# Performance work log

Hardware: AMD Instinct MI355X
Metric: run time of the kernel (lower is better)

Reference implementation:

```python
import jax, jax.numpy as jnp
import numpy as np

HEADS = 4
DIM_HEAD = 32


def setup_inputs() -> dict:
    key = jax.random.key(0)
    k1, k2, k3, k4 = jax.random.split(key, 4)
    x = jax.random.normal(k1, (2, 64, 48, 48, 48), dtype=jnp.float32)
    # 1x1x1 conv weights collapse to plain channel-mixing matrices
    w_qkv = jax.random.normal(k2, (384, 64), dtype=jnp.float32) * 0.05  # [3*heads*dh, dim]
    w_out = jax.random.normal(k3, (64, 128), dtype=jnp.float32) * 0.05  # [dim, heads*dh]
    b_out = jax.random.normal(k4, (64,), dtype=jnp.float32) * 0.05
    return {"x": x, "w_qkv": w_qkv, "w_out": w_out, "b_out": b_out}


def reference(x, w_qkv, w_out, b_out):
    b, c, D, H, W = x.shape
    N = D * H * W
    x_flat = x.reshape(b, c, N)
    # 1x1 conv == channel matmul: [b, 3*heads*dh, N]
    qkv = jnp.einsum('oc,bcn->bon', w_qkv, x_flat)
    # channel order: (qkv, heads, dh)
    qkv = qkv.reshape(b, 3, HEADS, DIM_HEAD, N)
    q, k, v = qkv[:, 0], qkv[:, 1], qkv[:, 2]
    k = jax.nn.softmax(k, axis=-1)  # softmax over the token axis N
    context = jnp.einsum('bhdn,bhen->bhde', k, v)   # [b, h, dh, dh]
    out = jnp.einsum('bhde,bhdn->bhen', context, q)  # [b, h, dh, N]
    out = out.reshape(b, HEADS * DIM_HEAD, N)
    y = jnp.einsum('oc,bcn->bon', w_out, out) + b_out[None, :, None]
    return y.reshape(b, c, D, H, W)
```

## Files before the change

### kernel.cpp

```cpp
#include <hip/hip_runtime.h>


#define C_IN 64
#define NREP 16

typedef __attribute__((ext_vector_type(8))) short short8;
typedef __attribute__((ext_vector_type(4))) float f32x4;

static __device__ __forceinline__ unsigned short f2bf(float f) {
    union { float f; unsigned u; } x; x.f = f;
    return (unsigned short)((x.u + 0x7fffu + ((x.u >> 16) & 1u)) >> 16);
}

__global__ __launch_bounds__(256)
void transpose_kernel(const float* __restrict__ x,
                      unsigned short* __restrict__ xT,
                      int N, int bbase)
{
    __shared__ float Xs[64][65];
    const int by = blockIdx.y;
    const int b  = by + bbase;
    const int t  = threadIdx.x;
    const int n0 = blockIdx.x * 64;

    const float* xb = x + (size_t)b * C_IN * N;
    #pragma unroll
    for (int i = 0; i < 4; ++i) {
        int slot = i * 256 + t;
        int c = slot >> 4, nq = slot & 15;
        float4 v = *(const float4*)(xb + (size_t)c * N + n0 + nq * 4);
        Xs[c][nq * 4 + 0] = v.x; Xs[c][nq * 4 + 1] = v.y;
        Xs[c][nq * 4 + 2] = v.z; Xs[c][nq * 4 + 3] = v.w;
    }
    __syncthreads();

    const int n = t >> 2, q = t & 3;
    unsigned out[8];
    #pragma unroll
    for (int i = 0; i < 8; ++i) {
        float lo = Xs[q * 16 + 2 * i][n], hi = Xs[q * 16 + 2 * i + 1][n];
        out[i] = (unsigned)f2bf(lo) | ((unsigned)f2bf(hi) << 16);
    }
    unsigned short* dst = xT + ((size_t)by * N + n0 + n) * 64 + q * 16;
    *(uint4*)(dst)     = *(uint4*)&out[0];
    *(uint4*)(dst + 8) = *(uint4*)&out[4];
}

__global__ __launch_bounds__(256, 3)
void kv_ctx_mfma(const unsigned short* __restrict__ xT,
                 const float* __restrict__ w_qkv,
                 float* __restrict__ ctx_acc,
                 float* __restrict__ s_acc,
                 int N, int bbase)
{
    __shared__ __align__(16) unsigned short PV[4][2][32][72];

    const int by  = blockIdx.y;
    const int b   = by + bbase;
    const int t   = threadIdx.x;
    const int w   = t >> 6;
    const int l   = t & 63;
    const int l15 = l & 15;
    const int lg  = l >> 4;
    const int rep = blockIdx.x & (NREP - 1);

    const int n_blk = blockIdx.x * 256;

    short8 Wf[4][2];
    #pragma unroll
    for (int nt = 0; nt < 4; ++nt) {
        const int row = (nt < 2) ? (128 + w * 32 + nt * 16 + l15)
                                 : (256 + w * 32 + (nt - 2) * 16 + l15);
        const float* wr = w_qkv + (size_t)row * C_IN;
        #pragma unroll
        for (int s = 0; s < 2; ++s) {
            #pragma unroll
            for (int j = 0; j < 8; ++j)
                Wf[nt][s][j] = (short)f2bf(wr[s * 32 + lg * 8 + j]);
        }
    }

    f32x4 acc2[2][2];
    #pragma unroll
    for (int dt = 0; dt < 2; ++dt)
        #pragma unroll
        for (int et = 0; et < 2; ++et)
            acc2[dt][et] = (f32x4){0.f, 0.f, 0.f, 0.f};
    float s_loc[2] = {0.f, 0.f};

    for (int it = 0; it < 4; ++it) {
        const int nb = n_blk + it * 64;
        const unsigned short* xr = xT + ((size_t)by * N + nb) * 64;

        short8 Af[4][2];
        #pragma unroll
        for (int mt = 0; mt < 4; ++mt)
            #pragma unroll
            for (int s = 0; s < 2; ++s)
                Af[mt][s] = *(const short8*)(xr + (size_t)(mt * 16 + l15) * 64
                                             + s * 32 + lg * 8);

        #pragma unroll
        for (int mt = 0; mt < 4; ++mt) {
            #pragma unroll
            for (int nt = 0; nt < 4; ++nt) {
                f32x4 a = (f32x4){0.f, 0.f, 0.f, 0.f};
                a = __builtin_amdgcn_mfma_f32_16x16x32_bf16(Af[mt][0], Wf[nt][0], a, 0, 0, 0);
                a = __builtin_amdgcn_mfma_f32_16x16x32_bf16(Af[mt][1], Wf[nt][1], a, 0, 0, 0);
                const int nl = mt * 16 + lg * 4;
                if (nt < 2) {
                    float e0 = __expf(a[0]), e1 = __expf(a[1]);
                    float e2 = __expf(a[2]), e3 = __expf(a[3]);
                    s_loc[nt] += (e0 + e1) + (e2 + e3);
                    uint2 p;
                    p.x = (unsigned)f2bf(e0) | ((unsigned)f2bf(e1) << 16);
                    p.y = (unsigned)f2bf(e2) | ((unsigned)f2bf(e3) << 16);
                    *(uint2*)&PV[w][0][nt * 16 + l15][nl] = p;
                } else {
                    uint2 p;
                    p.x = (unsigned)f2bf(a[0]) | ((unsigned)f2bf(a[1]) << 16);
                    p.y = (unsigned)f2bf(a[2]) | ((unsigned)f2bf(a[3]) << 16);
                    *(uint2*)&PV[w][1][(nt - 2) * 16 + l15][nl] = p;
                }
            }
        }

        #pragma unroll
        for (int ns = 0; ns < 2; ++ns) {
            short8 A2[2], B2[2];
            #pragma unroll
            for (int dt = 0; dt < 2; ++dt)
                A2[dt] = *(const short8*)&PV[w][0][dt * 16 + l15][ns * 32 + lg * 8];
            #pragma unroll
            for (int et = 0; et < 2; ++et)
                B2[et] = *(const short8*)&PV[w][1][et * 16 + l15][ns * 32 + lg * 8];
            #pragma unroll
            for (int dt = 0; dt < 2; ++dt)
                #pragma unroll
                for (int et = 0; et < 2; ++et)
                    acc2[dt][et] = __builtin_amdgcn_mfma_f32_16x16x32_bf16(
                        A2[dt], B2[et], acc2[dt][et], 0, 0, 0);
        }
    }

    float* cb = ctx_acc + (((size_t)b * NREP + rep) * 128 + w * 32) * 32;
    #pragma unroll
    for (int dt = 0; dt < 2; ++dt)
        #pragma unroll
        for (int et = 0; et < 2; ++et)
            #pragma unroll
            for (int r = 0; r < 4; ++r)
                atomicAdd(&cb[(dt * 16 + lg * 4 + r) * 32 + et * 16 + l15],
                          acc2[dt][et][r]);

    #pragma unroll
    for (int nt = 0; nt < 2; ++nt) {
        float s = s_loc[nt];
        s += __shfl_xor(s, 16);
        s += __shfl_xor(s, 32);
        if (lg == 0)
            atomicAdd(&s_acc[((size_t)b * NREP + rep) * 128 + w * 32 + nt * 16 + l15], s);
    }
}

__global__ __launch_bounds__(256)
void finalize_kernel(const float* __restrict__ ctx_acc,
                     const float* __restrict__ s_acc,
                     const float* __restrict__ w_qkv,
                     const float* __restrict__ w_out,
                     unsigned short* __restrict__ wf_bf)
{
    const int b = blockIdx.y;
    const int s = blockIdx.x;
    const int t = threadIdx.x;

    __shared__ float Wq[128][64];
    __shared__ float Ctx[128][36];
    __shared__ float Tt[128][68];
    __shared__ float WoS[8][128];
    __shared__ float Sinv[128];

    #pragma unroll
    for (int i = 0; i < 8; ++i) {
        int idx = i * 1024 + t * 4;
        *(float4*)&Wq[idx >> 6][idx & 63] = *(const float4*)(w_qkv + idx);
    }
    {
        int idx = t * 4;
        int o = idx >> 7, he = idx & 127;
        *(float4*)&WoS[o][he] = *(const float4*)(w_out + (size_t)(s * 8 + o) * 128 + he);
    }
    if (t < 128) {
        float ssum = 0.f;
        #pragma unroll
        for (int rep = 0; rep < NREP; ++rep)
            ssum += s_acc[((size_t)b * NREP + rep) * 128 + t];
        Sinv[t] = 1.0f / ssum;
    }
    float cacc[16];
    #pragma unroll
    for (int i = 0; i < 16; ++i) cacc[i] = 0.f;
    {
        const float* cb = ctx_acc + (size_t)b * NREP * 4096;
        for (int rep = 0; rep < NREP; ++rep) {
            #pragma unroll
            for (int i = 0; i < 16; ++i)
                cacc[i] += cb[(size_t)rep * 4096 + i * 256 + t];
        }
    }
    __syncthreads();

    #pragma unroll
    for (int i = 0; i < 16; ++i) {
        int idx = i * 256 + t;
        Ctx[idx >> 5][idx & 31] = cacc[i] * Sinv[idx >> 5];
    }
    __syncthreads();

    {
        const int he0 = (t >> 3) * 4;
        const int c0  = (t & 7) * 8;
        const int hh  = he0 >> 5;
        const int e0  = he0 & 31;
        float acc[4][8];
        #pragma unroll
        for (int j = 0; j < 4; ++j)
            #pragma unroll
            for (int k = 0; k < 8; ++k) acc[j][k] = 0.f;

        for (int d = 0; d < 32; ++d) {
            float4 cv = *(const float4*)&Ctx[hh * 32 + d][e0];
            float4 w0 = *(const float4*)&Wq[hh * 32 + d][c0];
            float4 w1 = *(const float4*)&Wq[hh * 32 + d][c0 + 4];
            float wv[8] = {w0.x, w0.y, w0.z, w0.w, w1.x, w1.y, w1.z, w1.w};
            float cvv[4] = {cv.x, cv.y, cv.z, cv.w};
            #pragma unroll
            for (int j = 0; j < 4; ++j)
                #pragma unroll
                for (int k = 0; k < 8; ++k)
                    acc[j][k] = fmaf(cvv[j], wv[k], acc[j][k]);
        }
        #pragma unroll
        for (int j = 0; j < 4; ++j) {
            *(float4*)&Tt[he0 + j][c0]     = make_float4(acc[j][0], acc[j][1], acc[j][2], acc[j][3]);
            *(float4*)&Tt[he0 + j][c0 + 4] = make_float4(acc[j][4], acc[j][5], acc[j][6], acc[j][7]);
        }
    }
    __syncthreads();

    {
        const int o = t >> 5;
        const int c = (t & 31) * 2;
        float a0 = 0.f, a1 = 0.f, b0 = 0.f, b1 = 0.f;
        #pragma unroll
        for (int he = 0; he < 128; he += 2) {
            float w0 = WoS[o][he], w1 = WoS[o][he + 1];
            float2 t0 = *(const float2*)&Tt[he][c];
            float2 t1 = *(const float2*)&Tt[he + 1][c];
            a0 = fmaf(w0, t0.x, a0); a1 = fmaf(w0, t0.y, a1);
            b0 = fmaf(w1, t1.x, b0); b1 = fmaf(w1, t1.y, b1);
        }
        unsigned short* dst = wf_bf + (size_t)b * 4096 + (size_t)(s * 8 + o) * 64 + c;
        dst[0] = f2bf(a0 + b0);
        dst[1] = f2bf(a1 + b1);
    }
}

__global__ __launch_bounds__(256)
void out_gemm_mfma(const unsigned short* __restrict__ xT,
                   const unsigned short* __restrict__ wf_bf,
                   const float* __restrict__ b_out,
                   float* __restrict__ y,
                   int N, int bbase)
{
    const int by  = blockIdx.y;
    const int b   = by + bbase;
    const int t   = threadIdx.x;
    const int w   = t >> 6;
    const int l   = t & 63;
    const int l15 = l & 15;
    const int lg  = l >> 4;
    const int nb  = blockIdx.x * 256 + w * 64;

    short8 Bf[4][2];
    const unsigned short* wb = wf_bf + (size_t)b * 4096;
    #pragma unroll
    for (int ot = 0; ot < 4; ++ot)
        #pragma unroll
        for (int s = 0; s < 2; ++s)
            Bf[ot][s] = *(const short8*)(wb + (size_t)(ot * 16 + l15) * 64
                                         + s * 32 + lg * 8);
    float bias[4];
    #pragma unroll
    for (int ot = 0; ot < 4; ++ot) bias[ot] = b_out[ot * 16 + l15];

    short8 Af[4][2];
    const unsigned short* xr = xT + ((size_t)by * N + nb) * 64;
    #pragma unroll
    for (int mt = 0; mt < 4; ++mt)
        #pragma unroll
        for (int s = 0; s < 2; ++s)
            Af[mt][s] = *(const short8*)(xr + (size_t)(mt * 16 + l15) * 64
                                         + s * 32 + lg * 8);

    float* yb = y + (size_t)b * C_IN * N;
    #pragma unroll
    for (int mt = 0; mt < 4; ++mt) {
        #pragma unroll
        for (int ot = 0; ot < 4; ++ot) {
            f32x4 a = (f32x4){0.f, 0.f, 0.f, 0.f};
            a = __builtin_amdgcn_mfma_f32_16x16x32_bf16(Af[mt][0], Bf[ot][0], a, 0, 0, 0);
            a = __builtin_amdgcn_mfma_f32_16x16x32_bf16(Af[mt][1], Bf[ot][1], a, 0, 0, 0);
            float4 v = make_float4(a[0] + bias[ot], a[1] + bias[ot],
                                   a[2] + bias[ot], a[3] + bias[ot]);
            *(float4*)(yb + (size_t)(ot * 16 + l15) * N + nb + mt * 16 + lg * 4) = v;
        }
    }
}

extern "C" void kernel_launch(void* const* d_in, const int* in_sizes, int n_in,
                              void* d_out, int out_size, void* d_ws, size_t ws_size,
                              hipStream_t stream)
{
    const float* x     = (const float*)d_in[0];
    const float* w_qkv = (const float*)d_in[1];
    const float* w_out = (const float*)d_in[2];
    const float* b_out = (const float*)d_in[3];
    float* y = (float*)d_out;

    const int B = 2;
    const int N = in_sizes[0] / (B * C_IN);

    const size_t xT_batch = (size_t)N * 64 * 2;
    const size_t acc_b    = (size_t)B * NREP * (4096 + 128) * 4;
    const size_t wf_b     = (size_t)B * 4096 * 2;
    const bool   full     = ws_size >= 2 * xT_batch + acc_b + wf_b;

    unsigned short* xT   = (unsigned short*)d_ws;
    char* p              = (char*)d_ws + (full ? 2 * xT_batch : xT_batch);
    float* ctx_acc       = (float*)p;
    float* s_acc         = ctx_acc + (size_t)B * NREP * 4096;
    unsigned short* wf_bf = (unsigned short*)(s_acc + (size_t)B * NREP * 128);

    hipMemsetAsync(ctx_acc, 0, acc_b, stream);

    if (full) {
        transpose_kernel<<<dim3(N / 64, B), 256, 0, stream>>>(x, xT, N, 0);
        kv_ctx_mfma<<<dim3(N / 256, B), 256, 0, stream>>>(xT, w_qkv, ctx_acc, s_acc, N, 0);
        finalize_kernel<<<dim3(8, B), 256, 0, stream>>>(ctx_acc, s_acc, w_qkv, w_out, wf_bf);
        out_gemm_mfma<<<dim3(N / 256, B), 256, 0, stream>>>(xT, wf_bf, b_out, y, N, 0);
    } else {
        for (int b = 0; b < B; ++b) {
            transpose_kernel<<<dim3(N / 64, 1), 256, 0, stream>>>(x, xT, N, b);
            kv_ctx_mfma<<<dim3(N / 256, 1), 256, 0, stream>>>(xT, w_qkv, ctx_acc, s_acc, N, b);
        }
        finalize_kernel<<<dim3(8, B), 256, 0, stream>>>(ctx_acc, s_acc, w_qkv, w_out, wf_bf);
        for (int b = 0; b < B; ++b) {
            transpose_kernel<<<dim3(N / 64, 1), 256, 0, stream>>>(x, xT, N, b);
            out_gemm_mfma<<<dim3(N / 256, 1), 256, 0, stream>>>(xT, wf_bf, b_out, y, N, b);
        }
    }
}
```

Before: 80.92 us.

## Fuse transpose into KV context kernel and replace atomics with partial-sum reduction

The fp32-to-bf16 transpose now happens inside the KV/context kernel: each 64-token tile is staged in shared memory, converted, fed to the MFMAs from LDS and also written to xT for the output GEMM. This removes a separate launch and the global re-read of xT. Global atomicAdd accumulation with a memset is replaced by per-block partial writes plus a separate reduce kernel. The cost is more shared memory and extra syncs per iteration, which cut occupancy (launch bound 3 to 2), and a larger partial buffer to read back.

```diff
diff --git a/kernel.cpp b/kernel.cpp
--- a/kernel.cpp
+++ b/kernel.cpp
@@ -2,7 +2,6 @@
 
 
 #define C_IN 64
-#define NREP 16
 
 typedef __attribute__((ext_vector_type(8))) short short8;
 typedef __attribute__((ext_vector_type(4))) float f32x4;
@@ -12,59 +11,28 @@
     return (unsigned short)((x.u + 0x7fffu + ((x.u >> 16) & 1u)) >> 16);
 }
 
-__global__ __launch_bounds__(256)
-void transpose_kernel(const float* __restrict__ x,
-                      unsigned short* __restrict__ xT,
-                      int N, int bbase)
-{
-    __shared__ float Xs[64][65];
-    const int by = blockIdx.y;
-    const int b  = by + bbase;
-    const int t  = threadIdx.x;
-    const int n0 = blockIdx.x * 64;
-
-    const float* xb = x + (size_t)b * C_IN * N;
-    #pragma unroll
-    for (int i = 0; i < 4; ++i) {
-        int slot = i * 256 + t;
-        int c = slot >> 4, nq = slot & 15;
-        float4 v = *(const float4*)(xb + (size_t)c * N + n0 + nq * 4);
-        Xs[c][nq * 4 + 0] = v.x; Xs[c][nq * 4 + 1] = v.y;
-        Xs[c][nq * 4 + 2] = v.z; Xs[c][nq * 4 + 3] = v.w;
-    }
-    __syncthreads();
-
-    const int n = t >> 2, q = t & 3;
-    unsigned out[8];
-    #pragma unroll
-    for (int i = 0; i < 8; ++i) {
-        float lo = Xs[q * 16 + 2 * i][n], hi = Xs[q * 16 + 2 * i + 1][n];
-        out[i] = (unsigned)f2bf(lo) | ((unsigned)f2bf(hi) << 16);
-    }
-    unsigned short* dst = xT + ((size_t)by * N + n0 + n) * 64 + q * 16;
-    *(uint4*)(dst)     = *(uint4*)&out[0];
-    *(uint4*)(dst + 8) = *(uint4*)&out[4];
-}
-
-__global__ __launch_bounds__(256, 3)
-void kv_ctx_mfma(const unsigned short* __restrict__ xT,
-                 const float* __restrict__ w_qkv,
-                 float* __restrict__ ctx_acc,
-                 float* __restrict__ s_acc,
-                 int N, int bbase)
-{
+__global__ __launch_bounds__(256, 2)
+void kv_ctx_fused(const float* __restrict__ x,
+                  const float* __restrict__ w_qkv,
+                  unsigned short* __restrict__ xT,
+                  float* __restrict__ part,
+                  int N, int nblk, int bbase)
+{
+    __shared__ float Xs[64][69];
+    __shared__ __align__(16) unsigned short Xbf[64][72];
     __shared__ __align__(16) unsigned short PV[4][2][32][72];
 
     const int by  = blockIdx.y;
     const int b   = by + bbase;
+    const int bx  = blockIdx.x;
     const int t   = threadIdx.x;
     const int w   = t >> 6;
     const int l   = t & 63;
     const int l15 = l & 15;
     const int lg  = l >> 4;
-    const int rep = blockIdx.x & (NREP - 1);
-
-    const int n_blk = blockIdx.x * 256;
+
+    const float* xb = x + (size_t)b * C_IN * N;
+    const int n_blk = bx * 256;
 
     short8 Wf[4][2];
     #pragma unroll
@@ -90,15 +58,40 @@
 
     for (int it = 0; it < 4; ++it) {
         const int nb = n_blk + it * 64;
-        const unsigned short* xr = xT + ((size_t)by * N + nb) * 64;
+        __syncthreads();
+
+        #pragma unroll
+        for (int i = 0; i < 4; ++i) {
+            int slot = i * 256 + t;
+            int c = slot >> 4, nq = slot & 15;
+            float4 v = *(const float4*)(xb + (size_t)c * N + nb + nq * 4);
+            Xs[c][nq * 4 + 0] = v.x; Xs[c][nq * 4 + 1] = v.y;
+            Xs[c][nq * 4 + 2] = v.z; Xs[c][nq * 4 + 3] = v.w;
+        }
+        __syncthreads();
+
+        {
+            const int n = t >> 2, q = t & 3;
+            unsigned out[8];
+            #pragma unroll
+            for (int i = 0; i < 8; ++i) {
+                float lo = Xs[q * 16 + 2 * i][n], hi = Xs[q * 16 + 2 * i + 1][n];
+                out[i] = (unsigned)f2bf(lo) | ((unsigned)f2bf(hi) << 16);
+            }
+            *(uint4*)&Xbf[n][q * 16]     = *(uint4*)&out[0];
+            *(uint4*)&Xbf[n][q * 16 + 8] = *(uint4*)&out[4];
+            unsigned short* dst = xT + ((size_t)by * N + nb + n) * 64 + q * 16;
+            *(uint4*)(dst)     = *(uint4*)&out[0];
+            *(uint4*)(dst + 8) = *(uint4*)&out[4];
+        }
+        __syncthreads();
 
         short8 Af[4][2];
         #pragma unroll
         for (int mt = 0; mt < 4; ++mt)
             #pragma unroll
             for (int s = 0; s < 2; ++s)
-                Af[mt][s] = *(const short8*)(xr + (size_t)(mt * 16 + l15) * 64
-                                             + s * 32 + lg * 8);
+                Af[mt][s] = *(const short8*)&Xbf[mt * 16 + l15][s * 32 + lg * 8];
 
         #pragma unroll
         for (int mt = 0; mt < 4; ++mt) {
@@ -143,15 +136,15 @@
         }
     }
 
-    float* cb = ctx_acc + (((size_t)b * NREP + rep) * 128 + w * 32) * 32;
+    float* pb = part + ((size_t)b * nblk + bx) * 4224;
     #pragma unroll
     for (int dt = 0; dt < 2; ++dt)
         #pragma unroll
         for (int et = 0; et < 2; ++et)
             #pragma unroll
             for (int r = 0; r < 4; ++r)
-                atomicAdd(&cb[(dt * 16 + lg * 4 + r) * 32 + et * 16 + l15],
-                          acc2[dt][et][r]);
+                pb[(w * 32 + dt * 16 + lg * 4 + r) * 32 + et * 16 + l15] =
+                    acc2[dt][et][r];
 
     #pragma unroll
     for (int nt = 0; nt < 2; ++nt) {
@@ -159,13 +152,33 @@
         s += __shfl_xor(s, 16);
         s += __shfl_xor(s, 32);
         if (lg == 0)
-            atomicAdd(&s_acc[((size_t)b * NREP + rep) * 128 + w * 32 + nt * 16 + l15], s);
+            pb[4096 + w * 32 + nt * 16 + l15] = s;
     }
 }
 
 __global__ __launch_bounds__(256)
-void finalize_kernel(const float* __restrict__ ctx_acc,
-                     const float* __restrict__ s_acc,
+void reduce_kernel(const float* __restrict__ part,
+                   float* __restrict__ red,
+                   int nblk)
+{
+    const int b = blockIdx.y;
+    const int g = blockIdx.x * 256 + threadIdx.x;
+    if (g >= 4224) return;
+    const float* pb = part + (size_t)b * nblk * 4224 + g;
+    float a0 = 0.f, a1 = 0.f, a2 = 0.f, a3 = 0.f;
+    int blk = 0;
+    for (; blk + 4 <= nblk; blk += 4) {
+        a0 += pb[(size_t)(blk + 0) * 4224];
+        a1 += pb[(size_t)(blk + 1) * 4224];
+        a2 += pb[(size_t)(blk + 2) * 4224];
+        a3 += pb[(size_t)(blk + 3) * 4224];
+    }
+    for (; blk < nblk; ++blk) a0 += pb[(size_t)blk * 4224];
+    red[(size_t)b * 4224 + g] = (a0 + a1) + (a2 + a3);
+}
+
+__global__ __launch_bounds__(256)
+void finalize_kernel(const float* __restrict__ red,
                      const float* __restrict__ w_qkv,
                      const float* __restrict__ w_out,
                      unsigned short* __restrict__ wf_bf)
@@ -190,30 +203,13 @@
         int o = idx >> 7, he = idx & 127;
         *(float4*)&WoS[o][he] = *(const float4*)(w_out + (size_t)(s * 8 + o) * 128 + he);
     }
-    if (t < 128) {
-        float ssum = 0.f;
-        #pragma unroll
-        for (int rep = 0; rep < NREP; ++rep)
-            ssum += s_acc[((size_t)b * NREP + rep) * 128 + t];
-        Sinv[t] = 1.0f / ssum;
-    }
-    float cacc[16];
-    #pragma unroll
-    for (int i = 0; i < 16; ++i) cacc[i] = 0.f;
-    {
-        const float* cb = ctx_acc + (size_t)b * NREP * 4096;
-        for (int rep = 0; rep < NREP; ++rep) {
-            #pragma unroll
-            for (int i = 0; i < 16; ++i)
-                cacc[i] += cb[(size_t)rep * 4096 + i * 256 + t];
-        }
-    }
+    if (t < 128) Sinv[t] = 1.0f / red[(size_t)b * 4224 + 4096 + t];
     __syncthreads();
 
     #pragma unroll
     for (int i = 0; i < 16; ++i) {
         int idx = i * 256 + t;
-        Ctx[idx >> 5][idx & 31] = cacc[i] * Sinv[idx >> 5];
+        Ctx[idx >> 5][idx & 31] = red[(size_t)b * 4224 + idx] * Sinv[idx >> 5];
     }
     __syncthreads();
 
@@ -318,6 +314,39 @@
     }
 }
 
+__global__ __launch_bounds__(256)
+void transpose_kernel(const float* __restrict__ x,
+                      unsigned short* __restrict__ xT,
+                      int N, int bbase)
+{
+    __shared__ float Xs[64][65];
+    const int b  = blockIdx.y + bbase;
+    const int t  = threadIdx.x;
+    const int n0 = blockIdx.x * 64;
+
+    const float* xb = x + (size_t)b * C_IN * N;
+    #pragma unroll
+    for (int i = 0; i < 4; ++i) {
+        int slot = i * 256 + t;
+        int c = slot >> 4, nq = slot & 15;
+        float4 v = *(const float4*)(xb + (size_t)c * N + n0 + nq * 4);
+        Xs[c][nq * 4 + 0] = v.x; Xs[c][nq * 4 + 1] = v.y;
+        Xs[c][nq * 4 + 2] = v.z; Xs[c][nq * 4 + 3] = v.w;
+    }
+    __syncthreads();
+
+    const int n = t >> 2, q = t & 3;
+    unsigned out[8];
+    #pragma unroll
+    for (int i = 0; i < 8; ++i) {
+        float lo = Xs[q * 16 + 2 * i][n], hi = Xs[q * 16 + 2 * i + 1][n];
+        out[i] = (unsigned)f2bf(lo) | ((unsigned)f2bf(hi) << 16);
+    }
+    unsigned short* dst = xT + ((size_t)blockIdx.y * N + n0 + n) * 64 + q * 16;
+    *(uint4*)(dst)     = *(uint4*)&out[0];
+    *(uint4*)(dst + 8) = *(uint4*)&out[4];
+}
+
 extern "C" void kernel_launch(void* const* d_in, const int* in_sizes, int n_in,
                               void* d_out, int out_size, void* d_ws, size_t ws_size,
                               hipStream_t stream)
@@ -330,34 +359,33 @@
 
     const int B = 2;
     const int N = in_sizes[0] / (B * C_IN);
+    const int nblk = N / 256;
 
     const size_t xT_batch = (size_t)N * 64 * 2;
-    const size_t acc_b    = (size_t)B * NREP * (4096 + 128) * 4;
+    const size_t part_b   = (size_t)B * nblk * 4224 * 4;
+    const size_t red_b    = (size_t)B * 4224 * 4;
     const size_t wf_b     = (size_t)B * 4096 * 2;
-    const bool   full     = ws_size >= 2 * xT_batch + acc_b + wf_b;
-
-    unsigned short* xT   = (unsigned short*)d_ws;
-    char* p              = (char*)d_ws + (full ? 2 * xT_batch : xT_batch);
-    float* ctx_acc       = (float*)p;
-    float* s_acc         = ctx_acc + (size_t)B * NREP * 4096;
-    unsigned short* wf_bf = (unsigned short*)(s_acc + (size_t)B * NREP * 128);
-
-    hipMemsetAsync(ctx_acc, 0, acc_b, stream);
+    const bool   full     = ws_size >= 2 * xT_batch + part_b + red_b + wf_b;
+
+    unsigned short* xT    = (unsigned short*)d_ws;
+    char* p               = (char*)d_ws + (full ? 2 * xT_batch : xT_batch);
+    float* part           = (float*)p;
+    float* red            = part + (size_t)B * nblk * 4224;
+    unsigned short* wf_bf = (unsigned short*)(red + (size_t)B * 4224);
 
     if (full) {
-        transpose_kernel<<<dim3(N / 64, B), 256, 0, stream>>>(x, xT, N, 0);
-        kv_ctx_mfma<<<dim3(N / 256, B), 256, 0, stream>>>(xT, w_qkv, ctx_acc, s_acc, N, 0);
-        finalize_kernel<<<dim3(8, B), 256, 0, stream>>>(ctx_acc, s_acc, w_qkv, w_out, wf_bf);
-        out_gemm_mfma<<<dim3(N / 256, B), 256, 0, stream>>>(xT, wf_bf, b_out, y, N, 0);
+        kv_ctx_fused<<<dim3(nblk, B), 256, 0, stream>>>(x, w_qkv, xT, part, N, nblk, 0);
+        reduce_kernel<<<dim3(17, B), 256, 0, stream>>>(part, red, nblk);
+        finalize_kernel<<<dim3(8, B), 256, 0, stream>>>(red, w_qkv, w_out, wf_bf);
+        out_gemm_mfma<<<dim3(nblk, B), 256, 0, stream>>>(xT, wf_bf, b_out, y, N, 0);
     } else {
+        for (int b = 0; b < B; ++b)
+            kv_ctx_fused<<<dim3(nblk, 1), 256, 0, stream>>>(x, w_qkv, xT, part, N, nblk, b);
+        reduce_kernel<<<dim3(17, B), 256, 0, stream>>>(part, red, nblk);
+        finalize_kernel<<<dim3(8, B), 256, 0, stream>>>(red, w_qkv, w_out, wf_bf);
         for (int b = 0; b < B; ++b) {
             transpose_kernel<<<dim3(N / 64, 1), 256, 0, stream>>>(x, xT, N, b);
-            kv_ctx_mfma<<<dim3(N / 256, 1), 256, 0, stream>>>(xT, w_qkv, ctx_acc, s_acc, N, b);
-        }
-        finalize_kernel<<<dim3(8, B), 256, 0, stream>>>(ctx_acc, s_acc, w_qkv, w_out, wf_bf);
-        for (int b = 0; b < B; ++b) {
-            transpose_kernel<<<dim3(N / 64, 1), 256, 0, stream>>>(x, xT, N, b);
-            out_gemm_mfma<<<dim3(N / 256, 1), 256, 0, stream>>>(xT, wf_bf, b_out, y, N, b);
-        }
-    }
-}
+            out_gemm_mfma<<<dim3(nblk, 1), 256, 0, stream>>>(xT, wf_bf, b_out, y, N, b);
+        }
+    }
+}
```

After: 96.59 us. 19.4% more time.
